# Performance work log

Measured on AMD Instinct MI355X. Metric: run time of the kernel, lower is better.

## Reference

```python
import jax, jax.numpy as jnp
import numpy as np

N = 50000      # nodes
E = 800000     # edges (before self loops)
IN = 256       # in_dim
HID = 64       # hidden_dim
H = 4          # heads
OUT = 32       # out_dim (latent); conv2 out_channels = 2*OUT
NEG_SLOPE = 0.2
EPS = 1e-5


def setup_inputs() -> dict:
    key = jax.random.key(0)
    ks = jax.random.split(key, 12)
    s = 0.05
    x = jax.random.normal(ks[0], (N, IN), dtype=jnp.float32)
    edge_index = jax.random.randint(ks[1], (2, E), 0, N, dtype=jnp.int64)
    # conv1: GATv2Conv(IN -> HID, heads=H, concat=True)
    W1l = jax.random.normal(ks[2], (IN, H * HID), dtype=jnp.float32) * s
    W1r = jax.random.normal(ks[3], (IN, H * HID), dtype=jnp.float32) * s
    att1 = jax.random.normal(ks[4], (H, HID), dtype=jnp.float32) * s
    b1 = jnp.zeros((H * HID,), dtype=jnp.float32)
    # BatchNorm1 (affine)
    g1 = jnp.ones((H * HID,), dtype=jnp.float32) + 0.1 * jax.random.normal(ks[5], (H * HID,), dtype=jnp.float32)
    be1 = 0.1 * jax.random.normal(ks[6], (H * HID,), dtype=jnp.float32)
    # conv2: GATv2Conv(H*HID -> 2*OUT, heads=H, concat=False)
    W2l = jax.random.normal(ks[7], (H * HID, H * 2 * OUT), dtype=jnp.float32) * s
    W2r = jax.random.normal(ks[8], (H * HID, H * 2 * OUT), dtype=jnp.float32) * s
    att2 = jax.random.normal(ks[9], (H, 2 * OUT), dtype=jnp.float32) * s
    b2 = jnp.zeros((2 * OUT,), dtype=jnp.float32)
    return {"x": x, "edge_index": edge_index, "W1l": W1l, "W1r": W1r,
            "att1": att1, "b1": b1, "g1": g1, "be1": be1,
            "W2l": W2l, "W2r": W2r, "att2": att2, "b2": b2}


def _gatv2(x, Wl, Wr, att, bias, src, dst, heads, ch, concat):
    # PyG GATv2Conv: xl = lin_l(x) (source side), xr = lin_r(x) (target side)
    xl = (x @ Wl).reshape(N, heads, ch)
    xr = (x @ Wr).reshape(N, heads, ch)
    e = jax.nn.leaky_relu(xl[src] + xr[dst], NEG_SLOPE)      # [E', H, C]
    score = jnp.einsum('ehc,hc->eh', e, att)                 # [E', H]
    # segment softmax over edges grouped by destination node
    m = jax.ops.segment_max(score, dst, num_segments=N)
    ex = jnp.exp(score - m[dst])
    den = jax.ops.segment_sum(ex, dst, num_segments=N)
    alpha = ex / den[dst]                                    # [E', H]
    out = jax.ops.segment_sum(alpha[..., None] * xl[src], dst, num_segments=N)  # [N, H, C]
    out = out.reshape(N, heads * ch) if concat else out.mean(axis=1)
    return out + bias


def _bn(x, gamma, beta):
    mu = x.mean(axis=0)
    var = x.var(axis=0)  # biased, as in nn.BatchNorm1d training mode
    xh = (x - mu) / jnp.sqrt(var + EPS)
    if gamma is None:
        return xh
    return xh * gamma + beta


def reference(x, edge_index, W1l, W1r, att1, b1, g1, be1, W2l, W2r, att2, b2):
    loops = jnp.arange(N, dtype=edge_index.dtype)
    src = jnp.concatenate([edge_index[0], loops])
    dst = jnp.concatenate([edge_index[1], loops])
    h = _gatv2(x, W1l, W1r, att1, b1, src, dst, H, HID, True)   # [N, H*HID]
    h = jax.nn.relu(_bn(h, g1, be1))
    o = _gatv2(h, W2l, W2r, att2, b2, src, dst, H, 2 * OUT, False)  # [N, 2*OUT]
    z_mu = _bn(o[:, :OUT], None, None)          # BatchNorm(affine=False)
    z_sig = jax.nn.sigmoid(o[:, OUT:])
    return (z_mu, z_sig)
```

## Files before the change

### kernel.cpp

```cpp
#include <hip/hip_runtime.h>
#include <math.h>

#define EPSBN 1e-5f

typedef __attribute__((ext_vector_type(8))) short short8;
typedef __attribute__((ext_vector_type(8))) _Float16 f16x8;
typedef __attribute__((ext_vector_type(2))) _Float16 h2;
typedef __attribute__((ext_vector_type(4))) float f32x4;

#if defined(__has_builtin)
#if __has_builtin(__builtin_amdgcn_fdot2)
#define HAVE_FDOT2 1
#endif
#endif

__device__ __forceinline__ unsigned short f2h(float f) {
  _Float16 h = (_Float16)f;
  return __builtin_bit_cast(unsigned short, h);
}
__device__ __forceinline__ h2 bch(unsigned u) { return __builtin_bit_cast(h2, u); }
__device__ __forceinline__ unsigned h2u(h2 v) { return __builtin_bit_cast(unsigned, v); }
__device__ __forceinline__ int swz(int b) { return b ^ (((b >> 7) & 3) << 4); }

__global__ __launch_bounds__(256) void gemm_dual(const unsigned short* __restrict__ Ab,
                                                 const unsigned short* __restrict__ Wt,
                                                 unsigned short* __restrict__ C, int M) {
  __shared__ __align__(16) short As[4096];
  __shared__ __align__(16) short Bs[4096];
  const int tid = threadIdx.x;
  const int lane = tid & 63, w = tid >> 6;
  const int wr = w >> 1, wc = w & 1;
  const int bm = blockIdx.x * 128, bn = blockIdx.y * 128;

  const int srow = tid >> 2;
  const int scol = (tid & 3) << 4;
  const char* gA = (const char*)Ab + (size_t)(bm + srow) * 512 + scol;
  const char* gB = (const char*)Wt + (size_t)(bn + srow) * 512 + scol;
  char* wA0 = (char*)As + swz(tid * 16);
  char* wA1 = (char*)As + swz((256 + tid) * 16);
  char* wB0 = (char*)Bs + swz(tid * 16);
  char* wB1 = (char*)Bs + swz((256 + tid) * 16);

  int aoff[4], boff[4];
#pragma unroll
  for (int i = 0; i < 4; ++i) {
    aoff[i] = swz(((wr * 64 + i * 16 + (lane & 15)) << 6) + ((lane >> 4) << 4));
    boff[i] = swz(((wc * 64 + i * 16 + (lane & 15)) << 6) + ((lane >> 4) << 4));
  }

  f32x4 acc[4][4] = {};
  short8 ra0 = *(const short8*)(gA);
  short8 ra1 = *(const short8*)(gA + 64 * 512);
  short8 rb0 = *(const short8*)(gB);
  short8 rb1 = *(const short8*)(gB + 64 * 512);

  for (int ks = 0; ks < 8; ++ks) {
    *(short8*)wA0 = ra0; *(short8*)wA1 = ra1;
    *(short8*)wB0 = rb0; *(short8*)wB1 = rb1;
    __syncthreads();
    if (ks < 7) {
      int off = (ks + 1) * 64;
      ra0 = *(const short8*)(gA + off);
      ra1 = *(const short8*)(gA + 64 * 512 + off);
      rb0 = *(const short8*)(gB + off);
      rb1 = *(const short8*)(gB + 64 * 512 + off);
    }
    short8 af[4], bfr[4];
#pragma unroll
    for (int i = 0; i < 4; ++i) af[i] = *(const short8*)((const char*)As + aoff[i]);
#pragma unroll
    for (int i = 0; i < 4; ++i) bfr[i] = *(const short8*)((const char*)Bs + boff[i]);
#pragma unroll
    for (int mr = 0; mr < 4; ++mr)
#pragma unroll
      for (int nc = 0; nc < 4; ++nc)
        acc[mr][nc] = __builtin_amdgcn_mfma_f32_16x16x32_f16(
            __builtin_bit_cast(f16x8, bfr[nc]), __builtin_bit_cast(f16x8, af[mr]),
            acc[mr][nc], 0, 0, 0);
    __syncthreads();
  }

#pragma unroll
  for (int mr = 0; mr < 4; ++mr) {
    int row = bm + wr * 64 + mr * 16 + (lane & 15);
    if (row < M) {
#pragma unroll
      for (int nc = 0; nc < 4; ++nc) {
        int col = bn + wc * 64 + nc * 16 + ((lane >> 4) << 2);
        ushort4 o;
        o.x = f2h(acc[mr][nc][0]); o.y = f2h(acc[mr][nc][1]);
        o.z = f2h(acc[mr][nc][2]); o.w = f2h(acc[mr][nc][3]);
        *(ushort4*)&C[(size_t)row * 512 + col] = o;
      }
    }
  }
}

__global__ void prep(const float* __restrict__ x, const float* __restrict__ W1l,
                     const float* __restrict__ W1r, const float* __restrict__ W2l,
                     const float* __restrict__ W2r, const int* __restrict__ ei,
                     unsigned short* __restrict__ xh, unsigned short* __restrict__ Wt1,
                     unsigned short* __restrict__ Wt2, int* __restrict__ cnt,
                     int n4x, int Etot, int E) {
  int t = blockIdx.x * 256 + threadIdx.x;
  if (t < n4x) {
    float4 v = *(const float4*)&x[(size_t)t * 4];
    ushort4 o;
    o.x = f2h(v.x); o.y = f2h(v.y); o.z = f2h(v.z); o.w = f2h(v.w);
    *(ushort4*)&xh[(size_t)t * 4] = o;
    return;
  }
  t -= n4x;
  if (t < 131072) {
    int n = t >> 8, k = t & 255;
    const float* W = (n < 256) ? W1l : W1r;
    Wt1[t] = f2h(W[k * 256 + (n & 255)]);
    return;
  }
  t -= 131072;
  if (t < 131072) {
    int n = t >> 8, k = t & 255;
    const float* W = (n < 256) ? W2l : W2r;
    Wt2[t] = f2h(W[k * 256 + (n & 255)]);
    return;
  }
  t -= 131072;
  if (t < Etot) {
    int d = (t < E) ? ei[E + t] : t - E;
    atomicAdd(&cnt[d], 1);
  }
}

__global__ __launch_bounds__(256) void scan_partial(const int* __restrict__ cnt,
                                                    int* __restrict__ bsum, int N) {
  __shared__ int red[256];
  int t = threadIdx.x;
  int i = blockIdx.x * 1024 + t * 4;
  int s = 0;
  if (i + 3 < N) {
    int4 v = *(const int4*)&cnt[i];
    s = v.x + v.y + v.z + v.w;
  } else {
    for (int k = 0; k < 4; ++k)
      if (i + k < N) s += cnt[i + k];
  }
  red[t] = s;
  __syncthreads();
  for (int off = 128; off > 0; off >>= 1) {
    if (t < off) red[t] += red[t + off];
    __syncthreads();
  }
  if (t == 0) bsum[blockIdx.x] = red[0];
}

__global__ void scan_bsums(const int* __restrict__ bsum, int* __restrict__ boff,
                           int* __restrict__ rowptr, int nb, int N, int Etot) {
  int t = threadIdx.x;
  int v = (t < nb) ? bsum[t] : 0;
  int x = v;
  for (int off = 1; off < 64; off <<= 1) {
    int y = __shfl_up(x, off);
    if (t >= off) x += y;
  }
  if (t < nb) boff[t] = x - v;
  if (t == 0) rowptr[N] = Etot;
}

__global__ __launch_bounds__(256) void scan_final(int* __restrict__ cnt,
                                                  const int* __restrict__ boff,
                                                  int* __restrict__ rowptr, int N) {
  __shared__ int red[256];
  int t = threadIdx.x;
  int i = blockIdx.x * 1024 + t * 4;
  int c0 = 0, c1 = 0, c2 = 0, c3 = 0;
  if (i + 3 < N) {
    int4 v = *(const int4*)&cnt[i];
    c0 = v.x; c1 = v.y; c2 = v.z; c3 = v.w;
    *(int4*)&cnt[i] = make_int4(0, 0, 0, 0);
  } else {
    if (i + 0 < N) { c0 = cnt[i + 0]; cnt[i + 0] = 0; }
    if (i + 1 < N) { c1 = cnt[i + 1]; cnt[i + 1] = 0; }
    if (i + 2 < N) { c2 = cnt[i + 2]; cnt[i + 2] = 0; }
    if (i + 3 < N) { c3 = cnt[i + 3]; cnt[i + 3] = 0; }
  }
  int s = c0 + c1 + c2 + c3;
  red[t] = s;
  __syncthreads();
  for (int off = 1; off < 256; off <<= 1) {
    int y = (t >= off) ? red[t - off] : 0;
    __syncthreads();
    red[t] += y;
    __syncthreads();
  }
  int excl = red[t] - s + boff[blockIdx.x];
  if (i + 3 < N) {
    *(int4*)&rowptr[i] = make_int4(excl, excl + c0, excl + c0 + c1, excl + c0 + c1 + c2);
  } else {
    if (i + 0 < N) rowptr[i + 0] = excl;
    if (i + 1 < N) rowptr[i + 1] = excl + c0;
    if (i + 2 < N) rowptr[i + 2] = excl + c0 + c1;
    if (i + 3 < N) rowptr[i + 3] = excl + c0 + c1 + c2;
  }
}

__global__ void scatter_src(const int* __restrict__ ei, const int* __restrict__ rowptr,
                            int* __restrict__ cur, int* __restrict__ srcs,
                            int Etot, int E) {
  int e = blockIdx.x * 256 + threadIdx.x;
  if (e >= Etot) return;
  int s, d;
  if (e < E) { s = ei[e]; d = ei[E + e]; } else { s = e - E; d = s; }
  int pos = rowptr[d] + atomicAdd(&cur[d], 1);
  srcs[pos] = s;
}

template <int CONCAT>
__global__ __launch_bounds__(256) void gat_fused(const unsigned short* __restrict__ xlr,
                                                 const float* __restrict__ att,
                                                 const float* __restrict__ bias,
                                                 const int* __restrict__ rowptr,
                                                 const int* __restrict__ srcs,
                                                 void* __restrict__ outv, int N) {
  int d = (blockIdx.x << 2) + (threadIdx.x >> 6);
  if (d >= N) return;
  int lane = threadIdx.x & 63;
  uint2 ub = *(const uint2*)&xlr[(size_t)d * 512 + 256 + lane * 4];
  h2 xb01 = bch(ub.x), xb23 = bch(ub.y);
  float4 wf = *(const float4*)&att[lane * 4];
  h2 w06a = {(_Float16)(0.6f * wf.x), (_Float16)(0.6f * wf.y)};
  h2 w06b = {(_Float16)(0.6f * wf.z), (_Float16)(0.6f * wf.w)};
  h2 w04a = {(_Float16)(0.4f * wf.x), (_Float16)(0.4f * wf.y)};
  h2 w04b = {(_Float16)(0.4f * wf.z), (_Float16)(0.4f * wf.w)};
  int i0 = rowptr[d], end = rowptr[d + 1];
  int eM1 = end - 1;
  float den = 0.f, a0 = 0.f, a1 = 0.f, a2 = 0.f, a3 = 0.f;

  auto GLD = [&](int j) -> uint2 {
    int jj = min(j, eM1);
    return *(const uint2*)&xlr[(size_t)srcs[jj] * 512 + lane * 4];
  };
  auto PROC = [&](uint2 cur) {
    h2 c01 = bch(cur.x), c23 = bch(cur.y);
    h2 e01 = c01 + xb01, e23 = c23 + xb23;
    float p;
#ifdef HAVE_FDOT2
    h2 ab01 = bch(h2u(e01) & 0x7FFF7FFFu);
    h2 ab23 = bch(h2u(e23) & 0x7FFF7FFFu);
    p = __builtin_amdgcn_fdot2(ab01, w04a,
        __builtin_amdgcn_fdot2(ab23, w04b,
        __builtin_amdgcn_fdot2(e01, w06a,
        __builtin_amdgcn_fdot2(e23, w06b, 0.f, false), false), false), false);
#else
    {
      float e0 = (float)e01.x, e1 = (float)e01.y, e2 = (float)e23.x, e3 = (float)e23.y;
      float l0 = fmaxf(e0, 0.2f * e0), l1 = fmaxf(e1, 0.2f * e1);
      float l2 = fmaxf(e2, 0.2f * e2), l3 = fmaxf(e3, 0.2f * e3);
      p = l0 * wf.x + l1 * wf.y + l2 * wf.z + l3 * wf.w;
    }
#endif
    p += __shfl_xor(p, 1);
    p += __shfl_xor(p, 2);
    p += __shfl_xor(p, 4);
    p += __shfl_xor(p, 8);
    float ex = __expf(p);
    den += ex;
    a0 = fmaf(ex, (float)c01.x, a0);
    a1 = fmaf(ex, (float)c01.y, a1);
    a2 = fmaf(ex, (float)c23.x, a2);
    a3 = fmaf(ex, (float)c23.y, a3);
  };

  uint2 b0 = GLD(i0), b1 = GLD(i0 + 1), b2 = GLD(i0 + 2), b3 = GLD(i0 + 3);
  for (int i = i0; i < end; i += 4) {
    uint2 c0 = b0, c1 = b1, c2 = b2, c3 = b3;
    b0 = GLD(i + 4); b1 = GLD(i + 5); b2 = GLD(i + 6); b3 = GLD(i + 7);
    PROC(c0);
    if (i + 1 < end) PROC(c1);
    if (i + 2 < end) PROC(c2);
    if (i + 3 < end) PROC(c3);
  }

  float inv = 1.f / den;
  if (CONCAT) {
    float4 bb = *(const float4*)&bias[lane * 4];
    ushort4 o;
    o.x = f2h(a0 * inv + bb.x); o.y = f2h(a1 * inv + bb.y);
    o.z = f2h(a2 * inv + bb.z); o.w = f2h(a3 * inv + bb.w);
    *(ushort4*)&((unsigned short*)outv)[(size_t)d * 256 + lane * 4] = o;
  } else {
    float v0 = a0 * inv, v1 = a1 * inv, v2 = a2 * inv, v3 = a3 * inv;
    v0 += __shfl_xor(v0, 16); v0 += __shfl_xor(v0, 32);
    v1 += __shfl_xor(v1, 16); v1 += __shfl_xor(v1, 32);
    v2 += __shfl_xor(v2, 16); v2 += __shfl_xor(v2, 32);
    v3 += __shfl_xor(v3, 16); v3 += __shfl_xor(v3, 32);
    if (lane < 16) {
      float4 bb = *(const float4*)&bias[lane * 4];
      *(float4*)&((float*)outv)[(size_t)d * 64 + lane * 4] =
          make_float4(0.25f * v0 + bb.x, 0.25f * v1 + bb.y,
                      0.25f * v2 + bb.z, 0.25f * v3 + bb.w);
    }
  }
}

__global__ __launch_bounds__(256) void bn_stats(const unsigned short* __restrict__ h,
                                                float* __restrict__ sums, int N) {
  __shared__ float4 rs[4][64], rq[4][64];
  int lane = threadIdx.x & 63;
  int rg = threadIdx.x >> 6;
  int c4 = lane * 4;
  float s0 = 0, s1 = 0, s2 = 0, s3 = 0, q0 = 0, q1 = 0, q2 = 0, q3 = 0;
  for (int r = blockIdx.x * 4 + rg; r < N; r += gridDim.x * 4) {
    uint2 v = *(const uint2*)&h[(size_t)r * 256 + c4];
    h2 a = bch(v.x), b = bch(v.y);
    float f0 = (float)a.x, f1 = (float)a.y, f2 = (float)b.x, f3 = (float)b.y;
    s0 += f0; q0 += f0 * f0;
    s1 += f1; q1 += f1 * f1;
    s2 += f2; q2 += f2 * f2;
    s3 += f3; q3 += f3 * f3;
  }
  rs[rg][lane] = make_float4(s0, s1, s2, s3);
  rq[rg][lane] = make_float4(q0, q1, q2, q3);
  __syncthreads();
  if (rg == 0) {
    float4 S = rs[0][lane], Q = rq[0][lane];
#pragma unroll
    for (int g = 1; g < 4; ++g) {
      float4 t = rs[g][lane]; S.x += t.x; S.y += t.y; S.z += t.z; S.w += t.w;
      float4 u = rq[g][lane]; Q.x += u.x; Q.y += u.y; Q.z += u.z; Q.w += u.w;
    }
    atomicAdd(&sums[c4 + 0], S.x); atomicAdd(&sums[c4 + 1], S.y);
    atomicAdd(&sums[c4 + 2], S.z); atomicAdd(&sums[c4 + 3], S.w);
    atomicAdd(&sums[256 + c4 + 0], Q.x); atomicAdd(&sums[256 + c4 + 1], Q.y);
    atomicAdd(&sums[256 + c4 + 2], Q.z); atomicAdd(&sums[256 + c4 + 3], Q.w);
  }
}

__global__ void bn_coef(const float* __restrict__ sums, const float* __restrict__ g,
                        const float* __restrict__ be, float* __restrict__ coef, int N) {
  int c = threadIdx.x;
  float inv_n = 1.f / (float)N;
  float mu = sums[c] * inv_n;
  float var = sums[256 + c] * inv_n - mu * mu;
  float sc = g[c] * rsqrtf(var + EPSBN);
  coef[c] = sc;
  coef[256 + c] = be[c] - mu * sc;
}

__global__ void bn_apply_relu(unsigned short* __restrict__ h, const float* __restrict__ coef,
                              int N) {
  int i = blockIdx.x * 256 + threadIdx.x;
  if (i >= N * 32) return;
  int base = i * 8, c = base & 255;
  uint4 v = *(const uint4*)&h[base];
  h2 p0 = bch(v.x), p1 = bch(v.y), p2 = bch(v.z), p3 = bch(v.w);
  float4 sA = *(const float4*)&coef[c];
  float4 sB = *(const float4*)&coef[c + 4];
  float4 hA = *(const float4*)&coef[256 + c];
  float4 hB = *(const float4*)&coef[256 + c + 4];
  float r0 = fmaf((float)p0.x, sA.x, hA.x); r0 = r0 > 0.f ? r0 : 0.f;
  float r1 = fmaf((float)p0.y, sA.y, hA.y); r1 = r1 > 0.f ? r1 : 0.f;
  float r2 = fmaf((float)p1.x, sA.z, hA.z); r2 = r2 > 0.f ? r2 : 0.f;
  float r3 = fmaf((float)p1.y, sA.w, hA.w); r3 = r3 > 0.f ? r3 : 0.f;
  float r4 = fmaf((float)p2.x, sB.x, hB.x); r4 = r4 > 0.f ? r4 : 0.f;
  float r5 = fmaf((float)p2.y, sB.y, hB.y); r5 = r5 > 0.f ? r5 : 0.f;
  float r6 = fmaf((float)p3.x, sB.z, hB.z); r6 = r6 > 0.f ? r6 : 0.f;
  float r7 = fmaf((float)p3.y, sB.w, hB.w); r7 = r7 > 0.f ? r7 : 0.f;
  uint4 o;
  o.x = (unsigned)f2h(r0) | ((unsigned)f2h(r1) << 16);
  o.y = (unsigned)f2h(r2) | ((unsigned)f2h(r3) << 16);
  o.z = (unsigned)f2h(r4) | ((unsigned)f2h(r5) << 16);
  o.w = (unsigned)f2h(r6) | ((unsigned)f2h(r7) << 16);
  *(uint4*)&h[base] = o;
}

__global__ __launch_bounds__(256) void bn2_stats(const float* __restrict__ o,
                                                 float* __restrict__ sums, int N) {
  __shared__ float4 lsum[256], lqum[256];
  int t = threadIdx.x;
  int q = t & 7, rs = t >> 3;
  float4 S = {0, 0, 0, 0}, Q = {0, 0, 0, 0};
  for (int r = blockIdx.x * 32 + rs; r < N; r += gridDim.x * 32) {
    float4 v = *(const float4*)&o[(size_t)r * 64 + q * 4];
    S.x += v.x; Q.x += v.x * v.x;
    S.y += v.y; Q.y += v.y * v.y;
    S.z += v.z; Q.z += v.z * v.z;
    S.w += v.w; Q.w += v.w * v.w;
  }
  lsum[t] = S; lqum[t] = Q;
  __syncthreads();
  if (t < 8) {
    float4 Sa = lsum[t], Qa = lqum[t];
    for (int k = 1; k < 32; ++k) {
      float4 a = lsum[t + 8 * k], b = lqum[t + 8 * k];
      Sa.x += a.x; Sa.y += a.y; Sa.z += a.z; Sa.w += a.w;
      Qa.x += b.x; Qa.y += b.y; Qa.z += b.z; Qa.w += b.w;
    }
    atomicAdd(&sums[t * 4 + 0], Sa.x); atomicAdd(&sums[t * 4 + 1], Sa.y);
    atomicAdd(&sums[t * 4 + 2], Sa.z); atomicAdd(&sums[t * 4 + 3], Sa.w);
    atomicAdd(&sums[32 + t * 4 + 0], Qa.x); atomicAdd(&sums[32 + t * 4 + 1], Qa.y);
    atomicAdd(&sums[32 + t * 4 + 2], Qa.z); atomicAdd(&sums[32 + t * 4 + 3], Qa.w);
  }
}

__global__ void write_out(const float* __restrict__ o, const float* __restrict__ sums,
                          float* __restrict__ out, int N) {
  int t = threadIdx.x;
  int n = blockIdx.x * 4 + (t >> 6);
  if (n >= N) return;
  int lane = t & 63;
  float v = o[(size_t)n * 64 + lane];
  if (lane < 32) {
    float inv_n = 1.f / (float)N;
    float mu = sums[lane] * inv_n;
    float var = sums[32 + lane] * inv_n - mu * mu;
    out[(size_t)n * 32 + lane] = (v - mu) * rsqrtf(var + EPSBN);
  } else {
    out[(size_t)N * 32 + (size_t)n * 32 + (lane - 32)] = 1.f / (1.f + __expf(-v));
  }
}

extern "C" void kernel_launch(void* const* d_in, const int* in_sizes, int n_in,
                              void* d_out, int out_size, void* d_ws, size_t ws_size,
                              hipStream_t stream) {
  const float* x    = (const float*)d_in[0];
  const int*   ei   = (const int*)d_in[1];
  const float* W1l  = (const float*)d_in[2];
  const float* W1r  = (const float*)d_in[3];
  const float* att1 = (const float*)d_in[4];
  const float* b1   = (const float*)d_in[5];
  const float* g1   = (const float*)d_in[6];
  const float* be1  = (const float*)d_in[7];
  const float* W2l  = (const float*)d_in[8];
  const float* W2r  = (const float*)d_in[9];
  const float* att2 = (const float*)d_in[10];
  const float* b2   = (const float*)d_in[11];
  float* out = (float*)d_out;

  const int N = in_sizes[0] / 256;
  const int E = in_sizes[1] / 2;
  const int Etot = E + N;
  const int Npad = ((N + 127) / 128) * 128;
  const int nb = (N + 1023) / 1024;

  char* ws = (char*)d_ws;
  unsigned short* xh  = (unsigned short*)ws; ws += (size_t)Npad * 256 * 2;
  unsigned short* hb  = (unsigned short*)ws; ws += (size_t)Npad * 256 * 2;
  unsigned short* AB  = (unsigned short*)ws; ws += (size_t)Npad * 512 * 2;
  unsigned short* Wt1 = (unsigned short*)ws; ws += (size_t)512 * 256 * 2;
  unsigned short* Wt2 = (unsigned short*)ws; ws += (size_t)512 * 256 * 2;
  float* o    = (float*)ws;  ws += (size_t)N * 64 * 4;
  int* rowptr = (int*)ws;    ws += (size_t)(N + 1) * 4;
  int* cnt    = (int*)ws;    ws += (size_t)N * 4;
  int* srcs   = (int*)ws;    ws += (size_t)Etot * 4;
  int* bsum   = (int*)ws;    ws += 64 * 4;
  int* boff   = (int*)ws;    ws += 64 * 4;
  float* sums1 = (float*)ws; ws += 512 * 4;
  float* sums2 = (float*)ws; ws += 64 * 4;
  float* coef1 = (float*)ws; ws += 512 * 4;

  dim3 gemmGrid(Npad / 128, 4);
  int dstBlocks = (N + 3) / 4;
  int n4x = N * 64;
  int prepTotal = n4x + 131072 + 131072 + Etot;

  hipMemsetAsync(cnt, 0, (size_t)N * 4, stream);
  hipMemsetAsync(sums1, 0, 512 * 4, stream);
  hipMemsetAsync(sums2, 0, 64 * 4, stream);
  prep<<<(prepTotal + 255) / 256, 256, 0, stream>>>(x, W1l, W1r, W2l, W2r, ei,
                                                    xh, Wt1, Wt2, cnt, n4x, Etot, E);
  scan_partial<<<nb, 256, 0, stream>>>(cnt, bsum, N);
  scan_bsums<<<1, 64, 0, stream>>>(bsum, boff, rowptr, nb, N, Etot);
  scan_final<<<nb, 256, 0, stream>>>(cnt, boff, rowptr, N);
  scatter_src<<<(Etot + 255) / 256, 256, 0, stream>>>(ei, rowptr, cnt, srcs, Etot, E);

  gemm_dual<<<gemmGrid, 256, 0, stream>>>(xh, Wt1, AB, N);
  gat_fused<1><<<dstBlocks, 256, 0, stream>>>(AB, att1, b1, rowptr, srcs, hb, N);
  bn_stats<<<512, 256, 0, stream>>>(hb, sums1, N);
  bn_coef<<<1, 256, 0, stream>>>(sums1, g1, be1, coef1, N);
  bn_apply_relu<<<(N * 32 + 255) / 256, 256, 0, stream>>>(hb, coef1, N);

  gemm_dual<<<gemmGrid, 256, 0, stream>>>(hb, Wt2, AB, N);
  gat_fused<0><<<dstBlocks, 256, 0, stream>>>(AB, att2, b2, rowptr, srcs, o, N);
  bn2_stats<<<128, 256, 0, stream>>>(o, sums2, N);
  write_out<<<dstBlocks, 256, 0, stream>>>(o, sums2, out, N);
}
```

Measured before the change: 517.0 us.

## Split wavefront into two edge streams in GAT aggregation and fold BN coef into apply

The GAT aggregation kernel now has each 64-lane wavefront handle two edges at once: each half-wave loads 8 fp16 channels per lane with 16-byte loads. The halves are combined with a cross-half shuffle at the end, and the per-head reduction is shortened accordingly. This aims to raise memory-level parallelism and load width on the gather-bound edge loop, at the cost of more registers and some wasted work on odd-degree nodes. Separately, the BN coefficient kernel is removed and each thread of the apply kernel recomputes scale and shift from the raw sums, saving one launch in exchange for redundant arithmetic.

```diff
diff --git a/kernel.cpp b/kernel.cpp
--- a/kernel.cpp
+++ b/kernel.cpp
@@ -224,80 +224,108 @@
   int d = (blockIdx.x << 2) + (threadIdx.x >> 6);
   if (d >= N) return;
   int lane = threadIdx.x & 63;
-  uint2 ub = *(const uint2*)&xlr[(size_t)d * 512 + 256 + lane * 4];
-  h2 xb01 = bch(ub.x), xb23 = bch(ub.y);
-  float4 wf = *(const float4*)&att[lane * 4];
-  h2 w06a = {(_Float16)(0.6f * wf.x), (_Float16)(0.6f * wf.y)};
-  h2 w06b = {(_Float16)(0.6f * wf.z), (_Float16)(0.6f * wf.w)};
-  h2 w04a = {(_Float16)(0.4f * wf.x), (_Float16)(0.4f * wf.y)};
-  h2 w04b = {(_Float16)(0.4f * wf.z), (_Float16)(0.4f * wf.w)};
+  int half = lane >> 5, sub = lane & 31;
+  uint4 ub = *(const uint4*)&xlr[(size_t)d * 512 + 256 + sub * 8];
+  h2 xb0 = bch(ub.x), xb1 = bch(ub.y), xb2 = bch(ub.z), xb3 = bch(ub.w);
+  float4 wa = *(const float4*)&att[sub * 8];
+  float4 wb = *(const float4*)&att[sub * 8 + 4];
+  h2 w060 = {(_Float16)(0.6f * wa.x), (_Float16)(0.6f * wa.y)};
+  h2 w061 = {(_Float16)(0.6f * wa.z), (_Float16)(0.6f * wa.w)};
+  h2 w062 = {(_Float16)(0.6f * wb.x), (_Float16)(0.6f * wb.y)};
+  h2 w063 = {(_Float16)(0.6f * wb.z), (_Float16)(0.6f * wb.w)};
+  h2 w040 = {(_Float16)(0.4f * wa.x), (_Float16)(0.4f * wa.y)};
+  h2 w041 = {(_Float16)(0.4f * wa.z), (_Float16)(0.4f * wa.w)};
+  h2 w042 = {(_Float16)(0.4f * wb.x), (_Float16)(0.4f * wb.y)};
+  h2 w043 = {(_Float16)(0.4f * wb.z), (_Float16)(0.4f * wb.w)};
   int i0 = rowptr[d], end = rowptr[d + 1];
   int eM1 = end - 1;
-  float den = 0.f, a0 = 0.f, a1 = 0.f, a2 = 0.f, a3 = 0.f;
-
-  auto GLD = [&](int j) -> uint2 {
-    int jj = min(j, eM1);
-    return *(const uint2*)&xlr[(size_t)srcs[jj] * 512 + lane * 4];
+  float den = 0.f;
+  float acc[8] = {};
+
+  auto GLD = [&](int e) -> uint4 {
+    int j = min(e + half, eM1);
+    return *(const uint4*)&xlr[(size_t)srcs[j] * 512 + sub * 8];
   };
-  auto PROC = [&](uint2 cur) {
-    h2 c01 = bch(cur.x), c23 = bch(cur.y);
-    h2 e01 = c01 + xb01, e23 = c23 + xb23;
+  uint4 bufA = GLD(i0), bufB = GLD(i0 + 2);
+  for (int i = i0; i < end; i += 2) {
+    uint4 c = bufA;
+    bufA = bufB;
+    bufB = GLD(i + 4);
+    h2 c0 = bch(c.x), c1 = bch(c.y), c2 = bch(c.z), c3 = bch(c.w);
+    h2 e0 = c0 + xb0, e1 = c1 + xb1, e2 = c2 + xb2, e3 = c3 + xb3;
     float p;
 #ifdef HAVE_FDOT2
-    h2 ab01 = bch(h2u(e01) & 0x7FFF7FFFu);
-    h2 ab23 = bch(h2u(e23) & 0x7FFF7FFFu);
-    p = __builtin_amdgcn_fdot2(ab01, w04a,
-        __builtin_amdgcn_fdot2(ab23, w04b,
-        __builtin_amdgcn_fdot2(e01, w06a,
-        __builtin_amdgcn_fdot2(e23, w06b, 0.f, false), false), false), false);
+    h2 a0 = bch(h2u(e0) & 0x7FFF7FFFu);
+    h2 a1 = bch(h2u(e1) & 0x7FFF7FFFu);
+    h2 a2 = bch(h2u(e2) & 0x7FFF7FFFu);
+    h2 a3 = bch(h2u(e3) & 0x7FFF7FFFu);
+    p = __builtin_amdgcn_fdot2(a0, w040,
+        __builtin_amdgcn_fdot2(a1, w041,
+        __builtin_amdgcn_fdot2(a2, w042,
+        __builtin_amdgcn_fdot2(a3, w043,
+        __builtin_amdgcn_fdot2(e0, w060,
+        __builtin_amdgcn_fdot2(e1, w061,
+        __builtin_amdgcn_fdot2(e2, w062,
+        __builtin_amdgcn_fdot2(e3, w063, 0.f, false), false), false), false),
+        false), false), false), false);
 #else
     {
-      float e0 = (float)e01.x, e1 = (float)e01.y, e2 = (float)e23.x, e3 = (float)e23.y;
-      float l0 = fmaxf(e0, 0.2f * e0), l1 = fmaxf(e1, 0.2f * e1);
-      float l2 = fmaxf(e2, 0.2f * e2), l3 = fmaxf(e3, 0.2f * e3);
-      p = l0 * wf.x + l1 * wf.y + l2 * wf.z + l3 * wf.w;
+      float f0 = (float)e0.x, f1 = (float)e0.y, f2 = (float)e1.x, f3 = (float)e1.y;
+      float f4 = (float)e2.x, f5 = (float)e2.y, f6 = (float)e3.x, f7 = (float)e3.y;
+      float l0 = fmaxf(f0, 0.2f * f0), l1 = fmaxf(f1, 0.2f * f1);
+      float l2 = fmaxf(f2, 0.2f * f2), l3 = fmaxf(f3, 0.2f * f3);
+      float l4 = fmaxf(f4, 0.2f * f4), l5 = fmaxf(f5, 0.2f * f5);
+      float l6 = fmaxf(f6, 0.2f * f6), l7 = fmaxf(f7, 0.2f * f7);
+      p = l0 * wa.x + l1 * wa.y + l2 * wa.z + l3 * wa.w +
+          l4 * wb.x + l5 * wb.y + l6 * wb.z + l7 * wb.w;
     }
 #endif
     p += __shfl_xor(p, 1);
     p += __shfl_xor(p, 2);
     p += __shfl_xor(p, 4);
-    p += __shfl_xor(p, 8);
-    float ex = __expf(p);
+    bool valid = (i + half) < end;
+    float ex = valid ? __expf(p) : 0.f;
     den += ex;
-    a0 = fmaf(ex, (float)c01.x, a0);
-    a1 = fmaf(ex, (float)c01.y, a1);
-    a2 = fmaf(ex, (float)c23.x, a2);
-    a3 = fmaf(ex, (float)c23.y, a3);
-  };
-
-  uint2 b0 = GLD(i0), b1 = GLD(i0 + 1), b2 = GLD(i0 + 2), b3 = GLD(i0 + 3);
-  for (int i = i0; i < end; i += 4) {
-    uint2 c0 = b0, c1 = b1, c2 = b2, c3 = b3;
-    b0 = GLD(i + 4); b1 = GLD(i + 5); b2 = GLD(i + 6); b3 = GLD(i + 7);
-    PROC(c0);
-    if (i + 1 < end) PROC(c1);
-    if (i + 2 < end) PROC(c2);
-    if (i + 3 < end) PROC(c3);
-  }
-
+    acc[0] = fmaf(ex, (float)c0.x, acc[0]);
+    acc[1] = fmaf(ex, (float)c0.y, acc[1]);
+    acc[2] = fmaf(ex, (float)c1.x, acc[2]);
+    acc[3] = fmaf(ex, (float)c1.y, acc[3]);
+    acc[4] = fmaf(ex, (float)c2.x, acc[4]);
+    acc[5] = fmaf(ex, (float)c2.y, acc[5]);
+    acc[6] = fmaf(ex, (float)c3.x, acc[6]);
+    acc[7] = fmaf(ex, (float)c3.y, acc[7]);
+  }
+  den += __shfl_xor(den, 32);
+#pragma unroll
+  for (int k = 0; k < 8; ++k) acc[k] += __shfl_xor(acc[k], 32);
   float inv = 1.f / den;
   if (CONCAT) {
-    float4 bb = *(const float4*)&bias[lane * 4];
-    ushort4 o;
-    o.x = f2h(a0 * inv + bb.x); o.y = f2h(a1 * inv + bb.y);
-    o.z = f2h(a2 * inv + bb.z); o.w = f2h(a3 * inv + bb.w);
-    *(ushort4*)&((unsigned short*)outv)[(size_t)d * 256 + lane * 4] = o;
+    if (half == 0) {
+      float4 ba = *(const float4*)&bias[sub * 8];
+      float4 bb2 = *(const float4*)&bias[sub * 8 + 4];
+      uint4 o;
+      o.x = (unsigned)f2h(fmaf(acc[0], inv, ba.x)) | ((unsigned)f2h(fmaf(acc[1], inv, ba.y)) << 16);
+      o.y = (unsigned)f2h(fmaf(acc[2], inv, ba.z)) | ((unsigned)f2h(fmaf(acc[3], inv, ba.w)) << 16);
+      o.z = (unsigned)f2h(fmaf(acc[4], inv, bb2.x)) | ((unsigned)f2h(fmaf(acc[5], inv, bb2.y)) << 16);
+      o.w = (unsigned)f2h(fmaf(acc[6], inv, bb2.z)) | ((unsigned)f2h(fmaf(acc[7], inv, bb2.w)) << 16);
+      *(uint4*)&((unsigned short*)outv)[(size_t)d * 256 + sub * 8] = o;
+    }
   } else {
-    float v0 = a0 * inv, v1 = a1 * inv, v2 = a2 * inv, v3 = a3 * inv;
-    v0 += __shfl_xor(v0, 16); v0 += __shfl_xor(v0, 32);
-    v1 += __shfl_xor(v1, 16); v1 += __shfl_xor(v1, 32);
-    v2 += __shfl_xor(v2, 16); v2 += __shfl_xor(v2, 32);
-    v3 += __shfl_xor(v3, 16); v3 += __shfl_xor(v3, 32);
-    if (lane < 16) {
-      float4 bb = *(const float4*)&bias[lane * 4];
-      *(float4*)&((float*)outv)[(size_t)d * 64 + lane * 4] =
-          make_float4(0.25f * v0 + bb.x, 0.25f * v1 + bb.y,
-                      0.25f * v2 + bb.z, 0.25f * v3 + bb.w);
+    float v[8];
+#pragma unroll
+    for (int k = 0; k < 8; ++k) {
+      v[k] = acc[k] * inv;
+      v[k] += __shfl_xor(v[k], 8);
+      v[k] += __shfl_xor(v[k], 16);
+    }
+    if (lane < 8) {
+      float4 ba = *(const float4*)&bias[sub * 8];
+      float4 bb2 = *(const float4*)&bias[sub * 8 + 4];
+      float* op = &((float*)outv)[(size_t)d * 64 + sub * 8];
+      *(float4*)op = make_float4(0.25f * v[0] + ba.x, 0.25f * v[1] + ba.y,
+                                 0.25f * v[2] + ba.z, 0.25f * v[3] + ba.w);
+      *(float4*)(op + 4) = make_float4(0.25f * v[4] + bb2.x, 0.25f * v[5] + bb2.y,
+                                       0.25f * v[6] + bb2.z, 0.25f * v[7] + bb2.w);
     }
   }
 }
@@ -335,41 +363,47 @@
   }
 }
 
-__global__ void bn_coef(const float* __restrict__ sums, const float* __restrict__ g,
-                        const float* __restrict__ be, float* __restrict__ coef, int N) {
-  int c = threadIdx.x;
-  float inv_n = 1.f / (float)N;
-  float mu = sums[c] * inv_n;
-  float var = sums[256 + c] * inv_n - mu * mu;
-  float sc = g[c] * rsqrtf(var + EPSBN);
-  coef[c] = sc;
-  coef[256 + c] = be[c] - mu * sc;
-}
-
-__global__ void bn_apply_relu(unsigned short* __restrict__ h, const float* __restrict__ coef,
+__global__ void bn_apply_relu(unsigned short* __restrict__ h, const float* __restrict__ sums,
+                              const float* __restrict__ g, const float* __restrict__ be,
                               int N) {
   int i = blockIdx.x * 256 + threadIdx.x;
   if (i >= N * 32) return;
   int base = i * 8, c = base & 255;
+  float inv_n = 1.f / (float)N;
+  float4 sm0 = *(const float4*)&sums[c],      sm1 = *(const float4*)&sums[c + 4];
+  float4 qm0 = *(const float4*)&sums[256 + c], qm1 = *(const float4*)&sums[256 + c + 4];
+  float4 gg0 = *(const float4*)&g[c],  gg1 = *(const float4*)&g[c + 4];
+  float4 bb0 = *(const float4*)&be[c], bb1 = *(const float4*)&be[c + 4];
+  float sc[8], sh[8];
+  float mus[8] = {sm0.x * inv_n, sm0.y * inv_n, sm0.z * inv_n, sm0.w * inv_n,
+                  sm1.x * inv_n, sm1.y * inv_n, sm1.z * inv_n, sm1.w * inv_n};
+  float qs[8] = {qm0.x * inv_n, qm0.y * inv_n, qm0.z * inv_n, qm0.w * inv_n,
+                 qm1.x * inv_n, qm1.y * inv_n, qm1.z * inv_n, qm1.w * inv_n};
+  float gv[8] = {gg0.x, gg0.y, gg0.z, gg0.w, gg1.x, gg1.y, gg1.z, gg1.w};
+  float bv[8] = {bb0.x, bb0.y, bb0.z, bb0.w, bb1.x, bb1.y, bb1.z, bb1.w};
+#pragma unroll
+  for (int k = 0; k < 8; ++k) {
+    sc[k] = gv[k] * rsqrtf(qs[k] - mus[k] * mus[k] + EPSBN);
+    sh[k] = bv[k] - mus[k] * sc[k];
+  }
   uint4 v = *(const uint4*)&h[base];
   h2 p0 = bch(v.x), p1 = bch(v.y), p2 = bch(v.z), p3 = bch(v.w);
-  float4 sA = *(const float4*)&coef[c];
-  float4 sB = *(const float4*)&coef[c + 4];
-  float4 hA = *(const float4*)&coef[256 + c];
-  float4 hB = *(const float4*)&coef[256 + c + 4];
-  float r0 = fmaf((float)p0.x, sA.x, hA.x); r0 = r0 > 0.f ? r0 : 0.f;
-  float r1 = fmaf((float)p0.y, sA.y, hA.y); r1 = r1 > 0.f ? r1 : 0.f;
-  float r2 = fmaf((float)p1.x, sA.z, hA.z); r2 = r2 > 0.f ? r2 : 0.f;
-  float r3 = fmaf((float)p1.y, sA.w, hA.w); r3 = r3 > 0.f ? r3 : 0.f;
-  float r4 = fmaf((float)p2.x, sB.x, hB.x); r4 = r4 > 0.f ? r4 : 0.f;
-  float r5 = fmaf((float)p2.y, sB.y, hB.y); r5 = r5 > 0.f ? r5 : 0.f;
-  float r6 = fmaf((float)p3.x, sB.z, hB.z); r6 = r6 > 0.f ? r6 : 0.f;
-  float r7 = fmaf((float)p3.y, sB.w, hB.w); r7 = r7 > 0.f ? r7 : 0.f;
+  float r[8];
+  r[0] = fmaf((float)p0.x, sc[0], sh[0]);
+  r[1] = fmaf((float)p0.y, sc[1], sh[1]);
+  r[2] = fmaf((float)p1.x, sc[2], sh[2]);
+  r[3] = fmaf((float)p1.y, sc[3], sh[3]);
+  r[4] = fmaf((float)p2.x, sc[4], sh[4]);
+  r[5] = fmaf((float)p2.y, sc[5], sh[5]);
+  r[6] = fmaf((float)p3.x, sc[6], sh[6]);
+  r[7] = fmaf((float)p3.y, sc[7], sh[7]);
+#pragma unroll
+  for (int k = 0; k < 8; ++k) r[k] = r[k] > 0.f ? r[k] : 0.f;
   uint4 o;
-  o.x = (unsigned)f2h(r0) | ((unsigned)f2h(r1) << 16);
-  o.y = (unsigned)f2h(r2) | ((unsigned)f2h(r3) << 16);
-  o.z = (unsigned)f2h(r4) | ((unsigned)f2h(r5) << 16);
-  o.w = (unsigned)f2h(r6) | ((unsigned)f2h(r7) << 16);
+  o.x = (unsigned)f2h(r[0]) | ((unsigned)f2h(r[1]) << 16);
+  o.y = (unsigned)f2h(r[2]) | ((unsigned)f2h(r[3]) << 16);
+  o.z = (unsigned)f2h(r[4]) | ((unsigned)f2h(r[5]) << 16);
+  o.w = (unsigned)f2h(r[6]) | ((unsigned)f2h(r[7]) << 16);
   *(uint4*)&h[base] = o;
 }
 
@@ -456,7 +490,6 @@
   int* boff   = (int*)ws;    ws += 64 * 4;
   float* sums1 = (float*)ws; ws += 512 * 4;
   float* sums2 = (float*)ws; ws += 64 * 4;
-  float* coef1 = (float*)ws; ws += 512 * 4;
 
   dim3 gemmGrid(Npad / 128, 4);
   int dstBlocks = (N + 3) / 4;
@@ -476,8 +509,7 @@
   gemm_dual<<<gemmGrid, 256, 0, stream>>>(xh, Wt1, AB, N);
   gat_fused<1><<<dstBlocks, 256, 0, stream>>>(AB, att1, b1, rowptr, srcs, hb, N);
   bn_stats<<<512, 256, 0, stream>>>(hb, sums1, N);
-  bn_coef<<<1, 256, 0, stream>>>(sums1, g1, be1, coef1, N);
-  bn_apply_relu<<<(N * 32 + 255) / 256, 256, 0, stream>>>(hb, coef1, N);
+  bn_apply_relu<<<(N * 32 + 255) / 256, 256, 0, stream>>>(hb, sums1, g1, be1, N);
 
   gemm_dual<<<gemmGrid, 256, 0, stream>>>(hb, Wt2, AB, N);
   gat_fused<0><<<dstBlocks, 256, 0, stream>>>(AB, att2, b2, rowptr, srcs, o, N);
```

Result: slower. 535.4 us (+3.6%).
